# Kernel tuning notes

Measured on AMD Instinct MI355X. Metric: run time of the kernel, lower is better.

The kernel has to match this reference:

```python
import jax, jax.numpy as jnp
import numpy as np

D = 1024  # centroid feature dim; also appears as the hardcoded 1024 in reshape(1024, L)


def _per_sample_loss(centroids_b, units_b, L, C):
    # centroids_b: (T, D) float; units_b: (T,) int; L: scalar int length; C: (K, D)
    # Faithful to torch: gathered = C[units_b[:L]]            -> (L, D)
    #                    true_c   = gathered.reshape(D, L)    (row-major reshape, NOT transpose)
    # true_c[i, t] = gathered.flat[i*L + t] = C[units_b[(i*L+t)//D], (i*L+t)%D]
    T = centroids_b.shape[0]
    i = jnp.arange(D, dtype=jnp.int32)[:, None]   # (D, 1)
    t = jnp.arange(T, dtype=jnp.int32)[None, :]   # (1, T)
    flat = i * L.astype(jnp.int32) + t            # (D, T)
    r = jnp.clip(flat // D, 0, T - 1)             # row into gathered (valid wherever t < L)
    c = flat % D                                  # column into gathered
    true_c = C[units_b[r], c]                     # (D, T) gather
    diff = jnp.abs(centroids_b.T - true_c)        # (D, T)
    col = diff.sum(axis=0)                        # (T,) sum over feature dim (torch sum(dim=0))
    mask = (jnp.arange(T) < L).astype(col.dtype)
    return (col * mask).sum() / L.astype(col.dtype)  # torch .mean() over L valid positions


def setup_inputs() -> dict:
    key = jax.random.key(0)
    k1, k2, k3, k4 = jax.random.split(key, 4)
    B, T, K = 16, 4096, 1024
    centroids = jax.random.normal(k1, (B, T, D), dtype=jnp.float32)
    units = jax.random.randint(k2, (B, T), 0, K, dtype=jnp.int32)
    unit_lengths = jax.random.randint(k3, (B,), 1, T + 1, dtype=jnp.int32)  # >=1 to avoid /0
    C = jax.random.normal(k4, (K, D), dtype=jnp.float32)  # kmeans codebook (learned constant)
    return {"centroids": centroids, "units": units, "unit_lengths": unit_lengths, "C": C}


def reference(centroids, units, unit_lengths, C):
    losses = jax.vmap(_per_sample_loss, in_axes=(0, 0, 0, None))(centroids, units, unit_lengths, C)
    return losses.mean()  # loss /= B
```

## Files before the change

### kernel.cpp

```cpp
#include <hip/hip_runtime.h>

#define FEAT_D 1024
#define TT 64
#define TI 64
#define PITCH 65

__global__ __launch_bounds__(256)
void centroid_loss_kernel(const float* __restrict__ centroids,
                          const int*   __restrict__ units,
                          const int*   __restrict__ unit_lengths,
                          const float* __restrict__ Cmat,
                          float*       __restrict__ out,
                          int B, int T)
{
    const int b  = blockIdx.y;
    const int t0 = blockIdx.x * TT;
    const int L  = unit_lengths[b];
    if (t0 >= L) return;

    __shared__ float tile[TT * PITCH];
    __shared__ float wsum[4];

    const int tid  = threadIdx.x;
    const int lane = tid & 63;
    const int wave = tid >> 6;
    const int t    = t0 + lane;
    const float valid = (t < L) ? 1.0f : 0.0f;

    const float* cent_b  = centroids + (size_t)b * T * FEAT_D;
    const int*   units_b = units + (size_t)b * T;

    float acc = 0.0f;

    for (int chunk = 0; chunk < FEAT_D / TI; ++chunk) {
        const int i0 = chunk * TI;

        {
            const int ii4  = tid & 15;
            const int trow = tid >> 4;
            #pragma unroll
            for (int p = 0; p < 4; ++p) {
                const int tt = trow + p * 16;
                const float4 v = *(const float4*)(cent_b + (size_t)(t0 + tt) * FEAT_D + i0 + ii4 * 4);
                float* dst = &tile[tt * PITCH + ii4 * 4];
                dst[0] = v.x; dst[1] = v.y; dst[2] = v.z; dst[3] = v.w;
            }
        }
        __syncthreads();

        const int ibase = i0 + wave * 16;
        #pragma unroll
        for (int k = 0; k < 16; ++k) {
            const int i    = ibase + k;
            const int flat = i * L + t;
            int r = flat >> 10;
            r = (r < T - 1) ? r : (T - 1);
            const int c = flat & 1023;
            const int u = units_b[r];
            const float cv = Cmat[u * FEAT_D + c];
            const float a  = tile[lane * PITCH + (i - i0)];
            acc += valid * fabsf(a - cv);
        }
        __syncthreads();
    }

    #pragma unroll
    for (int off = 32; off > 0; off >>= 1)
        acc += __shfl_down(acc, off, 64);
    if (lane == 0) wsum[wave] = acc;
    __syncthreads();
    if (tid == 0) {
        const float s = wsum[0] + wsum[1] + wsum[2] + wsum[3];
        atomicAdd(out, s / ((float)L * (float)B));
    }
}

extern "C" void kernel_launch(void* const* d_in, const int* in_sizes, int n_in,
                              void* d_out, int out_size, void* d_ws, size_t ws_size,
                              hipStream_t stream) {
    const float* centroids    = (const float*)d_in[0];
    const int*   units        = (const int*)d_in[1];
    const int*   unit_lengths = (const int*)d_in[2];
    const float* Cmat         = (const float*)d_in[3];
    float* out = (float*)d_out;

    const int B = in_sizes[2];
    const int T = in_sizes[1] / B;

    hipMemsetAsync(d_out, 0, sizeof(float), stream);

    dim3 grid((T + TT - 1) / TT, B);
    dim3 block(256);
    centroid_loss_kernel<<<grid, block, 0, stream>>>(centroids, units, unit_lengths,
                                                     Cmat, out, B, T);
}
```

Baseline: 365.4 us.

## Split feature chunks across grid and reduce partials in a second kernel

Each feature chunk becomes its own block (3D grid over tile, chunk and batch) instead of looping over 16 chunks inside one block. This removes the per-chunk barriers and raises the block count for latency hiding. Per-block results go to a workspace array that a single-block kernel sums deterministically, replacing the memset and global atomics when workspace allows. Shared-memory pitch changes to 68 so tile stores and reads can use float4, and masking is applied once at the end.

```diff
diff --git a/kernel.cpp b/kernel.cpp
--- a/kernel.cpp
+++ b/kernel.cpp
@@ -3,66 +3,71 @@
 #define FEAT_D 1024
 #define TT 64
 #define TI 64
-#define PITCH 65
+#define PITCH 68
 
 __global__ __launch_bounds__(256)
-void centroid_loss_kernel(const float* __restrict__ centroids,
-                          const int*   __restrict__ units,
-                          const int*   __restrict__ unit_lengths,
-                          const float* __restrict__ Cmat,
-                          float*       __restrict__ out,
-                          int B, int T)
+void centroid_loss_partial(const float* __restrict__ centroids,
+                           const int*   __restrict__ units,
+                           const int*   __restrict__ unit_lengths,
+                           const float* __restrict__ Cmat,
+                           float*       __restrict__ partials,
+                           float*       __restrict__ out_atomic,
+                           int B, int T, int use_atomic)
 {
-    const int b  = blockIdx.y;
-    const int t0 = blockIdx.x * TT;
-    const int L  = unit_lengths[b];
-    if (t0 >= L) return;
+    const int b     = blockIdx.z;
+    const int chunk = blockIdx.y;
+    const int t0    = blockIdx.x * TT;
+    const int L     = unit_lengths[b];
+    const int slot  = (b * gridDim.y + chunk) * gridDim.x + blockIdx.x;
 
-    __shared__ float tile[TT * PITCH];
+    if (t0 >= L) {
+        if (!use_atomic && threadIdx.x == 0) partials[slot] = 0.0f;
+        return;
+    }
+
+    __shared__ __align__(16) float tile[TT * PITCH];
     __shared__ float wsum[4];
 
     const int tid  = threadIdx.x;
     const int lane = tid & 63;
     const int wave = tid >> 6;
     const int t    = t0 + lane;
-    const float valid = (t < L) ? 1.0f : 0.0f;
 
     const float* cent_b  = centroids + (size_t)b * T * FEAT_D;
     const int*   units_b = units + (size_t)b * T;
+    const int i0 = chunk * TI;
+
+    {
+        const int ii4  = tid & 15;
+        const int trow = tid >> 4;
+        #pragma unroll
+        for (int p = 0; p < 4; ++p) {
+            const int tt = trow + p * 16;
+            const float4 v = *(const float4*)(cent_b + (size_t)(t0 + tt) * FEAT_D + i0 + ii4 * 4);
+            *(float4*)&tile[tt * PITCH + ii4 * 4] = v;
+        }
+    }
+    __syncthreads();
 
     float acc = 0.0f;
-
-    for (int chunk = 0; chunk < FEAT_D / TI; ++chunk) {
-        const int i0 = chunk * TI;
-
-        {
-            const int ii4  = tid & 15;
-            const int trow = tid >> 4;
-            #pragma unroll
-            for (int p = 0; p < 4; ++p) {
-                const int tt = trow + p * 16;
-                const float4 v = *(const float4*)(cent_b + (size_t)(t0 + tt) * FEAT_D + i0 + ii4 * 4);
-                float* dst = &tile[tt * PITCH + ii4 * 4];
-                dst[0] = v.x; dst[1] = v.y; dst[2] = v.z; dst[3] = v.w;
-            }
-        }
-        __syncthreads();
-
-        const int ibase = i0 + wave * 16;
+    const int ibase = i0 + wave * 16;
+    #pragma unroll
+    for (int m = 0; m < 4; ++m) {
+        const float4 a4 = *(const float4*)&tile[lane * PITCH + wave * 16 + m * 4];
         #pragma unroll
-        for (int k = 0; k < 16; ++k) {
-            const int i    = ibase + k;
+        for (int j = 0; j < 4; ++j) {
+            const int i    = ibase + m * 4 + j;
             const int flat = i * L + t;
             int r = flat >> 10;
             r = (r < T - 1) ? r : (T - 1);
             const int c = flat & 1023;
             const int u = units_b[r];
             const float cv = Cmat[u * FEAT_D + c];
-            const float a  = tile[lane * PITCH + (i - i0)];
-            acc += valid * fabsf(a - cv);
+            const float a  = (&a4.x)[j];
+            acc += fabsf(a - cv);
         }
-        __syncthreads();
     }
+    acc *= (t < L) ? 1.0f : 0.0f;
 
     #pragma unroll
     for (int off = 32; off > 0; off >>= 1)
@@ -70,9 +75,29 @@
     if (lane == 0) wsum[wave] = acc;
     __syncthreads();
     if (tid == 0) {
-        const float s = wsum[0] + wsum[1] + wsum[2] + wsum[3];
-        atomicAdd(out, s / ((float)L * (float)B));
+        float s = (wsum[0] + wsum[1] + wsum[2] + wsum[3]) / ((float)L * (float)B);
+        if (use_atomic) atomicAdd(out_atomic, s);
+        else            partials[slot] = s;
     }
+}
+
+__global__ __launch_bounds__(256)
+void reduce_partials(const float* __restrict__ partials,
+                     float* __restrict__ out, int n4)
+{
+    float s = 0.0f;
+    for (int idx = threadIdx.x; idx < n4; idx += 256) {
+        const float4 v = ((const float4*)partials)[idx];
+        s += (v.x + v.y) + (v.z + v.w);
+    }
+    #pragma unroll
+    for (int off = 32; off > 0; off >>= 1)
+        s += __shfl_down(s, off, 64);
+    __shared__ float ws[4];
+    const int lane = threadIdx.x & 63, wave = threadIdx.x >> 6;
+    if (lane == 0) ws[wave] = s;
+    __syncthreads();
+    if (threadIdx.x == 0) out[0] = (ws[0] + ws[1]) + (ws[2] + ws[3]);
 }
 
 extern "C" void kernel_launch(void* const* d_in, const int* in_sizes, int n_in,
@@ -87,10 +112,21 @@
     const int B = in_sizes[2];
     const int T = in_sizes[1] / B;
 
-    hipMemsetAsync(d_out, 0, sizeof(float), stream);
+    const int ntile  = (T + TT - 1) / TT;
+    const int nchunk = FEAT_D / TI;
+    const int nslots = ntile * nchunk * B;
 
-    dim3 grid((T + TT - 1) / TT, B);
+    dim3 grid(ntile, nchunk, B);
     dim3 block(256);
-    centroid_loss_kernel<<<grid, block, 0, stream>>>(centroids, units, unit_lengths,
-                                                     Cmat, out, B, T);
+
+    if (ws_size >= (size_t)nslots * sizeof(float)) {
+        float* partials = (float*)d_ws;
+        centroid_loss_partial<<<grid, block, 0, stream>>>(centroids, units, unit_lengths,
+                                                          Cmat, partials, out, B, T, 0);
+        reduce_partials<<<1, block, 0, stream>>>(partials, out, nslots / 4);
+    } else {
+        hipMemsetAsync(d_out, 0, sizeof(float), stream);
+        centroid_loss_partial<<<grid, block, 0, stream>>>(centroids, units, unit_lengths,
+                                                          Cmat, nullptr, out, B, T, 1);
+    }
 }
```

After: 340.1 us. 6.9% less time.
